# Kernel tuning notes

Measured on AMD Instinct MI355X. Metric: run time of the kernel, lower is better.

The kernel has to match this reference:

```python
import jax, jax.numpy as jnp
import numpy as np

D_MODEL = 1024
NUM_HEADS = 16
D_HEAD = D_MODEL // NUM_HEADS


def setup_inputs() -> dict:
    key = jax.random.key(0)
    ks = jax.random.split(key, 7)
    B, S = 2, 2048
    scale = 1.0 / np.sqrt(D_MODEL)
    return {
        "x": jax.random.normal(ks[0], (B, S, D_MODEL), dtype=jnp.float32),
        "attn_weights": jnp.zeros((1,), dtype=jnp.float32),  # unused in original forward
        "Wq": jax.random.normal(ks[1], (D_MODEL, D_MODEL), dtype=jnp.float32) * scale,
        "Wk": jax.random.normal(ks[2], (D_MODEL, D_MODEL), dtype=jnp.float32) * scale,
        "Wv": jax.random.normal(ks[3], (D_MODEL, D_MODEL), dtype=jnp.float32) * scale,
        "Wp": jax.random.normal(ks[4], (D_MODEL, D_MODEL), dtype=jnp.float32) * scale,
        "bp": jnp.zeros((D_MODEL,), dtype=jnp.float32),
    }


def reference(x, attn_weights, Wq, Wk, Wv, Wp, bp):
    B, S, D = x.shape
    H, Dh = NUM_HEADS, D_HEAD
    # torch Linear: y = x @ W.T  (weights stored [out, in])
    q = (x @ Wq.T).reshape(B, S, H, Dh).transpose(0, 2, 1, 3)  # [B,H,S,Dh]
    k = (x @ Wk.T).reshape(B, S, H, Dh).transpose(0, 2, 1, 3)
    v = (x @ Wv.T).reshape(B, S, H, Dh).transpose(0, 2, 1, 3)
    # NOTE: original module applies NO 1/sqrt(d) scaling
    scores = jnp.einsum("bhqd,bhkd->bhqk", q, k)
    weights = jax.nn.softmax(scores, axis=-1)  # dropout is inference no-op
    out = jnp.einsum("bhqk,bhkd->bhqd", weights, v)
    out = out.transpose(0, 2, 1, 3).reshape(B, S, D)
    return out @ Wp.T + bp
```

## Files before the change

### kernel.cpp

```cpp
#include <hip/hip_runtime.h>
#include <hip/hip_bf16.h>

#define D_MODEL 1024
#define NUM_HEADS 16
#define D_HEAD 64
#define BATCH 2
#define SEQ 2048
#define TOKENS (BATCH * SEQ)

typedef __attribute__((ext_vector_type(8))) short bf16x8;
typedef __attribute__((ext_vector_type(4))) float f32x4;
typedef __attribute__((ext_vector_type(2))) unsigned int uint2v;

typedef __attribute__((address_space(1))) const unsigned int as1_uint;
typedef __attribute__((address_space(3))) unsigned int as3_uint;

#define LOG2E 1.44269504088896340736f

static __device__ __forceinline__ unsigned short f2bf(float f) {
    unsigned int u = __builtin_bit_cast(unsigned int, f);
    u += 0x7fffu + ((u >> 16) & 1u);
    return (unsigned short)(u >> 16);
}

static __device__ __forceinline__ unsigned int pk2bf(float a, float b) {
    __hip_bfloat162 h = __float22bfloat162_rn(float2{a, b});
    unsigned int u;
    __builtin_memcpy(&u, &h, 4);
    return u;
}

static __device__ __forceinline__ float fast_exp2(float x) {
    return __builtin_amdgcn_exp2f(x);
}

__global__ __launch_bounds__(256) void convert_bf16(
    const float* __restrict__ x,  const float* __restrict__ Wq,
    const float* __restrict__ Wk, const float* __restrict__ Wv,
    const float* __restrict__ Wp,
    unsigned short* __restrict__ xb,  unsigned short* __restrict__ Wqb,
    unsigned short* __restrict__ Wkb, unsigned short* __restrict__ Wvb,
    unsigned short* __restrict__ Wpb)
{
    int v = blockIdx.x * 256 + threadIdx.x;
    const float* s;
    unsigned short* d;
    int off;
    if (v < (1 << 20)) { s = x; d = xb; off = v; }
    else {
        int u = v - (1 << 20);
        int w = u >> 18;
        off = u & ((1 << 18) - 1);
        s = (w == 0) ? Wq : (w == 1) ? Wk : (w == 2) ? Wv : Wp;
        d = (w == 0) ? Wqb : (w == 1) ? Wkb : (w == 2) ? Wvb : Wpb;
    }
    float4 f = ((const float4*)s)[off];
    ushort4 o = { f2bf(f.x), f2bf(f.y), f2bf(f.z), f2bf(f.w) };
    ((ushort4*)d)[off] = o;
}

__global__ __launch_bounds__(512) void qkv_gemm(
    const unsigned short* __restrict__ xb,
    const unsigned short* __restrict__ Wqb, const unsigned short* __restrict__ Wkb,
    const unsigned short* __restrict__ Wvb,
    unsigned short* __restrict__ Q, unsigned short* __restrict__ Kb,
    unsigned short* __restrict__ Vt)
{
    const int m0 = blockIdx.x * 128;
    const int n0 = blockIdx.y * 128;

    __shared__ __attribute__((aligned(16))) unsigned short sm[65536];

    const int t = threadIdx.x;
    const int wave = t >> 6, lane = t & 63;
    const int wm = (wave & 1) * 64, wn = (wave >> 1) * 32;
    const int l15 = lane & 15, quad = lane >> 4;
    const int sw = l15 & 7;

    const unsigned short* Wz[3] = { Wqb, Wkb, Wvb };

    f32x4 acc[3][4][2];
#pragma unroll
    for (int z = 0; z < 3; z++)
#pragma unroll
        for (int i = 0; i < 4; i++)
#pragma unroll
            for (int j = 0; j < 2; j++) acc[z][i][j] = (f32x4)0.f;

    auto stage = [&](int k0, int buf) {
#pragma unroll
        for (int i = 0; i < 2; i++) {
            int fbase = wave * 64 + i * 512;
            int f = fbase + lane;
            int row = f >> 3, cp = f & 7;
            int c = cp ^ (row & 7);
            int srcc = k0 + c * 8;
            __builtin_amdgcn_global_load_lds(
                (as1_uint*)&xb[(size_t)(m0 + row) * D_MODEL + srcc],
                (as3_uint*)&sm[buf * 32768 + fbase * 8], 16, 0, 0);
#pragma unroll
            for (int z = 0; z < 3; z++)
                __builtin_amdgcn_global_load_lds(
                    (as1_uint*)&Wz[z][(size_t)(n0 + row) * D_MODEL + srcc],
                    (as3_uint*)&sm[buf * 32768 + (1 + z) * 8192 + fbase * 8],
                    16, 0, 0);
        }
    };

    stage(0, 0);
    __syncthreads();

    int cur = 0;
    for (int k0 = 0; k0 < D_MODEL; k0 += 64) {
        if (k0 + 64 < D_MODEL) stage(k0 + 64, cur ^ 1);

        const unsigned short* lA = &sm[cur * 32768];
#pragma unroll
        for (int kk = 0; kk < 2; kk++) {
            const int cc = ((kk * 4 + quad) ^ sw) * 8;
            bf16x8 a[4];
#pragma unroll
            for (int mt = 0; mt < 4; mt++)
                a[mt] = *(const bf16x8*)&lA[(wm + mt * 16 + l15) * 64 + cc];
#pragma unroll
            for (int z = 0; z < 3; z++) {
                const unsigned short* lB = &sm[cur * 32768 + (1 + z) * 8192];
                bf16x8 b[2];
#pragma unroll
                for (int nt = 0; nt < 2; nt++)
                    b[nt] = *(const bf16x8*)&lB[(wn + nt * 16 + l15) * 64 + cc];
#pragma unroll
                for (int mt = 0; mt < 4; mt++)
#pragma unroll
                    for (int nt = 0; nt < 2; nt++)
                        acc[z][mt][nt] = __builtin_amdgcn_mfma_f32_16x16x32_bf16(
                            a[mt], b[nt], acc[z][mt][nt], 0, 0, 0);
            }
        }
        __syncthreads();
        cur ^= 1;
    }

#pragma unroll
    for (int mt = 0; mt < 4; mt++)
#pragma unroll
        for (int nt = 0; nt < 2; nt++)
#pragma unroll
            for (int r = 0; r < 4; r++) {
                int row = m0 + wm + mt * 16 + quad * 4 + r;
                int col = n0 + wn + nt * 16 + l15;
                Q[(size_t)row * D_MODEL + col]  = f2bf(acc[0][mt][nt][r] * LOG2E);
                Kb[(size_t)row * D_MODEL + col] = f2bf(acc[1][mt][nt][r]);
            }
    {
        const int b = m0 >> 11;
        const int srow = (m0 & 2047) + wm + quad * 4;
#pragma unroll
        for (int mt = 0; mt < 4; mt++)
#pragma unroll
            for (int nt = 0; nt < 2; nt++) {
                int col = n0 + wn + nt * 16 + l15;
                int h = col >> 6, dh = col & 63;
                ushort4 pk = { f2bf(acc[2][mt][nt][0]), f2bf(acc[2][mt][nt][1]),
                               f2bf(acc[2][mt][nt][2]), f2bf(acc[2][mt][nt][3]) };
                *(ushort4*)&Vt[(size_t)((b * 16 + h) * 64 + dh) * SEQ + srow + mt * 16] = pk;
            }
    }
}

__global__ __launch_bounds__(512, 4) void attn(
    const unsigned short* __restrict__ Q, const unsigned short* __restrict__ K,
    const unsigned short* __restrict__ Vt, unsigned short* __restrict__ O)
{
    const int q0 = blockIdx.x * 128;
    const int bh = blockIdx.y;
    const int b = bh >> 4, h = bh & 15;
    const size_t base = (size_t)b * SEQ * D_MODEL + (size_t)h * D_HEAD;
    const size_t baseV = (size_t)bh * D_HEAD * SEQ;

    __shared__ __attribute__((aligned(16))) char smem[40960];
    unsigned short* lK0 = (unsigned short*)&smem[0];
    unsigned short* lV0 = (unsigned short*)&smem[16384];

    const int t = threadIdx.x;
    const int wave = t >> 6, lane = t & 63;
    const int l15 = lane & 15, quad = lane >> 4;
    const int wq = wave & 3;
    const int sh = wave >> 2;
    const int qw = q0 + wq * 32;
    const int sbase = sh * (SEQ / 2);

    unsigned short* lK  = lK0 + sh * 4096;
    unsigned short* lVt = lV0 + sh * 4096;

    bf16x8 ones;
#pragma unroll
    for (int i = 0; i < 8; i++) ones[i] = (short)0x3F80;

    bf16x8 bq[2][2];
#pragma unroll
    for (int mq = 0; mq < 2; mq++)
#pragma unroll
        for (int kk = 0; kk < 2; kk++)
            bq[mq][kk] = *(const bf16x8*)&Q[base +
                (size_t)(qw + mq * 16 + l15) * D_MODEL + kk * 32 + quad * 8];

    const int tl = t & 255;
    const int r0 = tl >> 3, c0 = tl & 7;
    const int cs = (c0 ^ (r0 & 7)) * 8;
    const unsigned short* gK0 = &K[base + (size_t)(sbase + r0) * D_MODEL + c0 * 8];
    const unsigned short* gK1 = &K[base + (size_t)(sbase + r0 + 32) * D_MODEL + c0 * 8];
    const unsigned short* gV0 = &Vt[baseV + (size_t)r0 * SEQ + sbase + c0 * 8];
    const unsigned short* gV1 = &Vt[baseV + (size_t)(r0 + 32) * SEQ + sbase + c0 * 8];

    const int sw = l15 & 7;

    f32x4 o_acc[2][4];
#pragma unroll
    for (int i = 0; i < 2; i++)
#pragma unroll
        for (int j = 0; j < 4; j++) o_acc[i][j] = (f32x4)0.f;
    f32x4 o_l[2];
#pragma unroll
    for (int i = 0; i < 2; i++) o_l[i] = (f32x4)0.f;

    uint4 rK0 = *(const uint4*)gK0;
    uint4 rK1 = *(const uint4*)gK1;
    uint4 rV0 = *(const uint4*)gV0;
    uint4 rV1 = *(const uint4*)gV1;

    for (int s0 = 0; s0 < SEQ / 2; s0 += 64) {
        __syncthreads();
        *(uint4*)&lK[r0 * 64 + cs]        = rK0;
        *(uint4*)&lK[(r0 + 32) * 64 + cs] = rK1;
        *(uint4*)&lVt[r0 * 64 + cs]        = rV0;
        *(uint4*)&lVt[(r0 + 32) * 64 + cs] = rV1;
        __syncthreads();

        int sn = (s0 + 64 < SEQ / 2) ? s0 + 64 : 0;
        rK0 = *(const uint4*)(gK0 + (size_t)sn * D_MODEL);
        rK1 = *(const uint4*)(gK1 + (size_t)sn * D_MODEL);
        rV0 = *(const uint4*)(gV0 + sn);
        rV1 = *(const uint4*)(gV1 + sn);

        f32x4 st[4][2];
#pragma unroll
        for (int mt = 0; mt < 4; mt++)
#pragma unroll
            for (int mq = 0; mq < 2; mq++) st[mt][mq] = (f32x4)0.f;
#pragma unroll
        for (int kk = 0; kk < 2; kk++) {
            const int cc = ((kk * 4 + quad) ^ sw) * 8;
#pragma unroll
            for (int mt = 0; mt < 4; mt++) {
                bf16x8 ak = *(const bf16x8*)&lK[(mt * 16 + l15) * 64 + cc];
#pragma unroll
                for (int mq = 0; mq < 2; mq++)
                    st[mt][mq] = __builtin_amdgcn_mfma_f32_16x16x32_bf16(
                        ak, bq[mq][kk], st[mt][mq], 0, 0, 0);
            }
        }

#pragma unroll
        for (int mq = 0; mq < 2; mq++)
#pragma unroll
            for (int mt = 0; mt < 4; mt++)
#pragma unroll
                for (int r = 0; r < 4; r++)
                    st[mt][mq][r] = fast_exp2(st[mt][mq][r]);

        bf16x8 pa[2][2];
#pragma unroll
        for (int mq = 0; mq < 2; mq++)
#pragma unroll
            for (int kk = 0; kk < 2; kk++) {
                unsigned int cw[4];
#pragma unroll
                for (int j = 0; j < 2; j++) {
                    unsigned int w0 = pk2bf(st[2 * kk][mq][2 * j],
                                            st[2 * kk][mq][2 * j + 1]);
                    unsigned int w1 = pk2bf(st[2 * kk + 1][mq][2 * j],
                                            st[2 * kk + 1][mq][2 * j + 1]);
                    uint2v uv = __builtin_amdgcn_permlane32_swap(w0, w1, false, false);
                    uint2v f  = __builtin_amdgcn_permlane16_swap(uv[0], uv[1], false, false);
                    cw[j]     = f[0];
                    cw[2 + j] = f[1];
                }
                union { unsigned int w[4]; bf16x8 v; } u;
                u.w[0] = cw[0]; u.w[1] = cw[1]; u.w[2] = cw[2]; u.w[3] = cw[3];
                pa[mq][kk] = u.v;
            }

#pragma unroll
        for (int kk = 0; kk < 2; kk++) {
            const int cc = ((kk * 4 + quad) ^ sw) * 8;
            bf16x8 bv[4];
#pragma unroll
            for (int nt = 0; nt < 4; nt++)
                bv[nt] = *(const bf16x8*)&lVt[(nt * 16 + l15) * 64 + cc];
#pragma unroll
            for (int mq = 0; mq < 2; mq++) {
#pragma unroll
                for (int nt = 0; nt < 4; nt++)
                    o_acc[mq][nt] = __builtin_amdgcn_mfma_f32_16x16x32_bf16(
                        pa[mq][kk], bv[nt], o_acc[mq][nt], 0, 0, 0);
                o_l[mq] = __builtin_amdgcn_mfma_f32_16x16x32_bf16(
                    pa[mq][kk], ones, o_l[mq], 0, 0, 0);
            }
        }
    }

    float* sO = (float*)&smem[0];
    float* sL = (float*)&smem[36864];
    __syncthreads();
    if (sh == 1) {
#pragma unroll
        for (int mq = 0; mq < 2; mq++) {
#pragma unroll
            for (int r = 0; r < 4; r++)
                sL[wq * 32 + mq * 16 + quad * 4 + r] = o_l[mq][r];
#pragma unroll
            for (int nt = 0; nt < 4; nt++)
#pragma unroll
                for (int r = 0; r < 4; r++)
                    sO[(wq * 32 + mq * 16 + quad * 4 + r) * 68 + nt * 16 + l15] =
                        o_acc[mq][nt][r];
        }
    }
    __syncthreads();
    if (sh == 0) {
#pragma unroll
        for (int mq = 0; mq < 2; mq++) {
            float inv[4];
#pragma unroll
            for (int r = 0; r < 4; r++)
                inv[r] = 1.f / (o_l[mq][r] + sL[wq * 32 + mq * 16 + quad * 4 + r]);
#pragma unroll
            for (int nt = 0; nt < 4; nt++)
#pragma unroll
                for (int r = 0; r < 4; r++) {
                    int row = qw + mq * 16 + quad * 4 + r;
                    float v = o_acc[mq][nt][r] +
                              sO[(wq * 32 + mq * 16 + quad * 4 + r) * 68 + nt * 16 + l15];
                    O[base + (size_t)row * D_MODEL + nt * 16 + l15] = f2bf(v * inv[r]);
                }
        }
    }
}

__global__ __launch_bounds__(512) void proj_gemm(
    const unsigned short* __restrict__ A, const unsigned short* __restrict__ W,
    const float* __restrict__ bias, float* __restrict__ out)
{
    const int m0 = blockIdx.x * 128;
    const int n0 = blockIdx.y * 128;

    __shared__ __attribute__((aligned(16))) unsigned short lA[128 * 64];
    __shared__ __attribute__((aligned(16))) unsigned short lB[128 * 64];

    const int t = threadIdx.x;
    const int wave = t >> 6, lane = t & 63;
    const int wm = (wave & 1) * 64, wn = (wave >> 1) * 32;
    const int l15 = lane & 15, quad = lane >> 4;
    const int sw = l15 & 7;

    f32x4 acc[4][2];
#pragma unroll
    for (int i = 0; i < 4; i++)
#pragma unroll
        for (int j = 0; j < 2; j++) acc[i][j] = (f32x4)0.f;

    for (int k0 = 0; k0 < D_MODEL; k0 += 64) {
        __syncthreads();
#pragma unroll
        for (int i = 0; i < 2; i++) {
            int fbase = wave * 64 + i * 512;
            int f = fbase + lane;
            int row = f >> 3, cp = f & 7;
            int c = cp ^ (row & 7);
            __builtin_amdgcn_global_load_lds(
                (as1_uint*)&A[(size_t)(m0 + row) * D_MODEL + k0 + c * 8],
                (as3_uint*)&lA[fbase * 8], 16, 0, 0);
            __builtin_amdgcn_global_load_lds(
                (as1_uint*)&W[(size_t)(n0 + row) * D_MODEL + k0 + c * 8],
                (as3_uint*)&lB[fbase * 8], 16, 0, 0);
        }
        __syncthreads();

#pragma unroll
        for (int kk = 0; kk < 2; kk++) {
            const int cc = ((kk * 4 + quad) ^ sw) * 8;
            bf16x8 a[4], b[2];
#pragma unroll
            for (int mt = 0; mt < 4; mt++)
                a[mt] = *(const bf16x8*)&lA[(wm + mt * 16 + l15) * 64 + cc];
#pragma unroll
            for (int nt = 0; nt < 2; nt++)
                b[nt] = *(const bf16x8*)&lB[(wn + nt * 16 + l15) * 64 + cc];
#pragma unroll
            for (int mt = 0; mt < 4; mt++)
#pragma unroll
                for (int nt = 0; nt < 2; nt++)
                    acc[mt][nt] = __builtin_amdgcn_mfma_f32_16x16x32_bf16(
                        a[mt], b[nt], acc[mt][nt], 0, 0, 0);
        }
    }

#pragma unroll
    for (int mt = 0; mt < 4; mt++)
#pragma unroll
        for (int nt = 0; nt < 2; nt++)
#pragma unroll
            for (int r = 0; r < 4; r++) {
                int row = m0 + wm + mt * 16 + quad * 4 + r;
                int col = n0 + wn + nt * 16 + l15;
                out[(size_t)row * D_MODEL + col] = acc[mt][nt][r] + bias[col];
            }
}

extern "C" void kernel_launch(void* const* d_in, const int* in_sizes, int n_in,
                              void* d_out, int out_size, void* d_ws, size_t ws_size,
                              hipStream_t stream)
{
    const float* x  = (const float*)d_in[0];
    const float* Wq = (const float*)d_in[2];
    const float* Wk = (const float*)d_in[3];
    const float* Wv = (const float*)d_in[4];
    const float* Wp = (const float*)d_in[5];
    const float* bp = (const float*)d_in[6];
    float* out = (float*)d_out;

    unsigned short* Q   = (unsigned short*)d_ws;
    unsigned short* K   = Q   + (size_t)TOKENS * D_MODEL;
    unsigned short* Vt  = K   + (size_t)TOKENS * D_MODEL;
    unsigned short* O   = Vt  + (size_t)TOKENS * D_MODEL;
    unsigned short* xb  = O   + (size_t)TOKENS * D_MODEL;
    unsigned short* Wqb = xb  + (size_t)TOKENS * D_MODEL;
    unsigned short* Wkb = Wqb + (size_t)D_MODEL * D_MODEL;
    unsigned short* Wvb = Wkb + (size_t)D_MODEL * D_MODEL;
    unsigned short* Wpb = Wvb + (size_t)D_MODEL * D_MODEL;

    convert_bf16<<<8192, 256, 0, stream>>>(x, Wq, Wk, Wv, Wp,
                                           xb, Wqb, Wkb, Wvb, Wpb);
    qkv_gemm<<<dim3(TOKENS / 128, D_MODEL / 128), 512, 0, stream>>>(
        xb, Wqb, Wkb, Wvb, Q, K, Vt);
    attn<<<dim3(SEQ / 128, BATCH * NUM_HEADS), 512, 0, stream>>>(Q, K, Vt, O);
    proj_gemm<<<dim3(TOKENS / 128, D_MODEL / 128), 512, 0, stream>>>(O, Wpb, bp, out);
}
```

Baseline: 179.9 us.

## Halve GEMM N-tile to 64 and double-buffer proj_gemm loads

Both the QKV and output-projection GEMMs now use 128x64 tiles instead of 128x128. This doubles the grid to 512 blocks and cuts LDS and accumulator registers per block, so more blocks can fit on each CU (launch bounds of 4). proj_gemm also gets a double-buffered global_load_lds pipeline like qkv_gemm, which overlaps the next K-slice load with the current MFMAs. The trade-off is lower arithmetic intensity per block, so the A tile is reloaded twice as often.

```diff
diff --git a/kernel.cpp b/kernel.cpp
--- a/kernel.cpp
+++ b/kernel.cpp
@@ -59,7 +59,7 @@
     ((ushort4*)d)[off] = o;
 }
 
-__global__ __launch_bounds__(512) void qkv_gemm(
+__global__ __launch_bounds__(512, 4) void qkv_gemm(
     const unsigned short* __restrict__ xb,
     const unsigned short* __restrict__ Wqb, const unsigned short* __restrict__ Wkb,
     const unsigned short* __restrict__ Wvb,
@@ -67,25 +67,23 @@
     unsigned short* __restrict__ Vt)
 {
     const int m0 = blockIdx.x * 128;
-    const int n0 = blockIdx.y * 128;
-
-    __shared__ __attribute__((aligned(16))) unsigned short sm[65536];
+    const int n0 = blockIdx.y * 64;
+
+    __shared__ __attribute__((aligned(16))) unsigned short sm[40960];
 
     const int t = threadIdx.x;
     const int wave = t >> 6, lane = t & 63;
-    const int wm = (wave & 1) * 64, wn = (wave >> 1) * 32;
+    const int wm = (wave & 1) * 64, wn = (wave >> 1) * 16;
     const int l15 = lane & 15, quad = lane >> 4;
     const int sw = l15 & 7;
 
     const unsigned short* Wz[3] = { Wqb, Wkb, Wvb };
 
-    f32x4 acc[3][4][2];
+    f32x4 acc[3][4];
 #pragma unroll
     for (int z = 0; z < 3; z++)
 #pragma unroll
-        for (int i = 0; i < 4; i++)
-#pragma unroll
-            for (int j = 0; j < 2; j++) acc[z][i][j] = (f32x4)0.f;
+        for (int i = 0; i < 4; i++) acc[z][i] = (f32x4)0.f;
 
     auto stage = [&](int k0, int buf) {
 #pragma unroll
@@ -94,15 +92,19 @@
             int f = fbase + lane;
             int row = f >> 3, cp = f & 7;
             int c = cp ^ (row & 7);
-            int srcc = k0 + c * 8;
             __builtin_amdgcn_global_load_lds(
-                (as1_uint*)&xb[(size_t)(m0 + row) * D_MODEL + srcc],
-                (as3_uint*)&sm[buf * 32768 + fbase * 8], 16, 0, 0);
+                (as1_uint*)&xb[(size_t)(m0 + row) * D_MODEL + k0 + c * 8],
+                (as3_uint*)&sm[buf * 20480 + fbase * 8], 16, 0, 0);
+        }
+        {
+            int row = t >> 3, cp = t & 7;
+            int c = cp ^ (row & 7);
+            int fbase = wave * 64;
 #pragma unroll
             for (int z = 0; z < 3; z++)
                 __builtin_amdgcn_global_load_lds(
-                    (as1_uint*)&Wz[z][(size_t)(n0 + row) * D_MODEL + srcc],
-                    (as3_uint*)&sm[buf * 32768 + (1 + z) * 8192 + fbase * 8],
+                    (as1_uint*)&Wz[z][(size_t)(n0 + row) * D_MODEL + k0 + c * 8],
+                    (as3_uint*)&sm[buf * 20480 + 8192 + z * 4096 + fbase * 8],
                     16, 0, 0);
         }
     };
@@ -114,7 +116,7 @@
     for (int k0 = 0; k0 < D_MODEL; k0 += 64) {
         if (k0 + 64 < D_MODEL) stage(k0 + 64, cur ^ 1);
 
-        const unsigned short* lA = &sm[cur * 32768];
+        const unsigned short* lA = &sm[cur * 20480];
 #pragma unroll
         for (int kk = 0; kk < 2; kk++) {
             const int cc = ((kk * 4 + quad) ^ sw) * 8;
@@ -124,17 +126,12 @@
                 a[mt] = *(const bf16x8*)&lA[(wm + mt * 16 + l15) * 64 + cc];
 #pragma unroll
             for (int z = 0; z < 3; z++) {
-                const unsigned short* lB = &sm[cur * 32768 + (1 + z) * 8192];
-                bf16x8 b[2];
-#pragma unroll
-                for (int nt = 0; nt < 2; nt++)
-                    b[nt] = *(const bf16x8*)&lB[(wn + nt * 16 + l15) * 64 + cc];
+                const unsigned short* lB = &sm[cur * 20480 + 8192 + z * 4096];
+                bf16x8 b = *(const bf16x8*)&lB[(wn + l15) * 64 + cc];
 #pragma unroll
                 for (int mt = 0; mt < 4; mt++)
-#pragma unroll
-                    for (int nt = 0; nt < 2; nt++)
-                        acc[z][mt][nt] = __builtin_amdgcn_mfma_f32_16x16x32_bf16(
-                            a[mt], b[nt], acc[z][mt][nt], 0, 0, 0);
+                    acc[z][mt] = __builtin_amdgcn_mfma_f32_16x16x32_bf16(
+                        a[mt], b, acc[z][mt], 0, 0, 0);
             }
         }
         __syncthreads();
@@ -144,27 +141,23 @@
 #pragma unroll
     for (int mt = 0; mt < 4; mt++)
 #pragma unroll
-        for (int nt = 0; nt < 2; nt++)
-#pragma unroll
-            for (int r = 0; r < 4; r++) {
-                int row = m0 + wm + mt * 16 + quad * 4 + r;
-                int col = n0 + wn + nt * 16 + l15;
-                Q[(size_t)row * D_MODEL + col]  = f2bf(acc[0][mt][nt][r] * LOG2E);
-                Kb[(size_t)row * D_MODEL + col] = f2bf(acc[1][mt][nt][r]);
-            }
+        for (int r = 0; r < 4; r++) {
+            int row = m0 + wm + mt * 16 + quad * 4 + r;
+            int col = n0 + wn + l15;
+            Q[(size_t)row * D_MODEL + col]  = f2bf(acc[0][mt][r] * LOG2E);
+            Kb[(size_t)row * D_MODEL + col] = f2bf(acc[1][mt][r]);
+        }
     {
         const int b = m0 >> 11;
         const int srow = (m0 & 2047) + wm + quad * 4;
-#pragma unroll
-        for (int mt = 0; mt < 4; mt++)
-#pragma unroll
-            for (int nt = 0; nt < 2; nt++) {
-                int col = n0 + wn + nt * 16 + l15;
-                int h = col >> 6, dh = col & 63;
-                ushort4 pk = { f2bf(acc[2][mt][nt][0]), f2bf(acc[2][mt][nt][1]),
-                               f2bf(acc[2][mt][nt][2]), f2bf(acc[2][mt][nt][3]) };
-                *(ushort4*)&Vt[(size_t)((b * 16 + h) * 64 + dh) * SEQ + srow + mt * 16] = pk;
-            }
+        const int h = n0 >> 6;
+        const int dh = wn + l15;
+#pragma unroll
+        for (int mt = 0; mt < 4; mt++) {
+            ushort4 pk = { f2bf(acc[2][mt][0]), f2bf(acc[2][mt][1]),
+                           f2bf(acc[2][mt][2]), f2bf(acc[2][mt][3]) };
+            *(ushort4*)&Vt[(size_t)((b * 16 + h) * 64 + dh) * SEQ + srow + mt * 16] = pk;
+        }
     }
 }
 
@@ -348,30 +341,26 @@
     }
 }
 
-__global__ __launch_bounds__(512) void proj_gemm(
+__global__ __launch_bounds__(512, 4) void proj_gemm(
     const unsigned short* __restrict__ A, const unsigned short* __restrict__ W,
     const float* __restrict__ bias, float* __restrict__ out)
 {
     const int m0 = blockIdx.x * 128;
-    const int n0 = blockIdx.y * 128;
-
-    __shared__ __attribute__((aligned(16))) unsigned short lA[128 * 64];
-    __shared__ __attribute__((aligned(16))) unsigned short lB[128 * 64];
+    const int n0 = blockIdx.y * 64;
+
+    __shared__ __attribute__((aligned(16))) unsigned short sm[24576];
 
     const int t = threadIdx.x;
     const int wave = t >> 6, lane = t & 63;
-    const int wm = (wave & 1) * 64, wn = (wave >> 1) * 32;
+    const int wm = (wave & 1) * 64, wn = (wave >> 1) * 16;
     const int l15 = lane & 15, quad = lane >> 4;
     const int sw = l15 & 7;
 
-    f32x4 acc[4][2];
-#pragma unroll
-    for (int i = 0; i < 4; i++)
-#pragma unroll
-        for (int j = 0; j < 2; j++) acc[i][j] = (f32x4)0.f;
-
-    for (int k0 = 0; k0 < D_MODEL; k0 += 64) {
-        __syncthreads();
+    f32x4 acc[4];
+#pragma unroll
+    for (int i = 0; i < 4; i++) acc[i] = (f32x4)0.f;
+
+    auto stage = [&](int k0, int buf) {
 #pragma unroll
         for (int i = 0; i < 2; i++) {
             int fbase = wave * 64 + i * 512;
@@ -380,42 +369,53 @@
             int c = cp ^ (row & 7);
             __builtin_amdgcn_global_load_lds(
                 (as1_uint*)&A[(size_t)(m0 + row) * D_MODEL + k0 + c * 8],
-                (as3_uint*)&lA[fbase * 8], 16, 0, 0);
+                (as3_uint*)&sm[buf * 12288 + fbase * 8], 16, 0, 0);
+        }
+        {
+            int row = t >> 3, cp = t & 7;
+            int c = cp ^ (row & 7);
+            int fbase = wave * 64;
             __builtin_amdgcn_global_load_lds(
                 (as1_uint*)&W[(size_t)(n0 + row) * D_MODEL + k0 + c * 8],
-                (as3_uint*)&lB[fbase * 8], 16, 0, 0);
-        }
-        __syncthreads();
-
+                (as3_uint*)&sm[buf * 12288 + 8192 + fbase * 8], 16, 0, 0);
+        }
+    };
+
+    stage(0, 0);
+    __syncthreads();
+
+    int cur = 0;
+    for (int k0 = 0; k0 < D_MODEL; k0 += 64) {
+        if (k0 + 64 < D_MODEL) stage(k0 + 64, cur ^ 1);
+
+        const unsigned short* lA = &sm[cur * 12288];
+        const unsigned short* lB = &sm[cur * 12288 + 8192];
 #pragma unroll
         for (int kk = 0; kk < 2; kk++) {
             const int cc = ((kk * 4 + quad) ^ sw) * 8;
-            bf16x8 a[4], b[2];
+            bf16x8 a[4];
 #pragma unroll
             for (int mt = 0; mt < 4; mt++)
                 a[mt] = *(const bf16x8*)&lA[(wm + mt * 16 + l15) * 64 + cc];
-#pragma unroll
-            for (int nt = 0; nt < 2; nt++)
-                b[nt] = *(const bf16x8*)&lB[(wn + nt * 16 + l15) * 64 + cc];
+            bf16x8 b = *(const bf16x8*)&lB[(wn + l15) * 64 + cc];
 #pragma unroll
             for (int mt = 0; mt < 4; mt++)
-#pragma unroll
-                for (int nt = 0; nt < 2; nt++)
-                    acc[mt][nt] = __builtin_amdgcn_mfma_f32_16x16x32_bf16(
-                        a[mt], b[nt], acc[mt][nt], 0, 0, 0);
-        }
-    }
-
+                acc[mt] = __builtin_amdgcn_mfma_f32_16x16x32_bf16(
+                    a[mt], b, acc[mt], 0, 0, 0);
+        }
+        __syncthreads();
+        cur ^= 1;
+    }
+
+    const int col = n0 + wn + l15;
+    const float bc = bias[col];
 #pragma unroll
     for (int mt = 0; mt < 4; mt++)
 #pragma unroll
-        for (int nt = 0; nt < 2; nt++)
-#pragma unroll
-            for (int r = 0; r < 4; r++) {
-                int row = m0 + wm + mt * 16 + quad * 4 + r;
-                int col = n0 + wn + nt * 16 + l15;
-                out[(size_t)row * D_MODEL + col] = acc[mt][nt][r] + bias[col];
-            }
+        for (int r = 0; r < 4; r++) {
+            int row = m0 + wm + mt * 16 + quad * 4 + r;
+            out[(size_t)row * D_MODEL + col] = acc[mt][r] + bc;
+        }
 }
 
 extern "C" void kernel_launch(void* const* d_in, const int* in_sizes, int n_in,
@@ -442,8 +442,8 @@
 
     convert_bf16<<<8192, 256, 0, stream>>>(x, Wq, Wk, Wv, Wp,
                                            xb, Wqb, Wkb, Wvb, Wpb);
-    qkv_gemm<<<dim3(TOKENS / 128, D_MODEL / 128), 512, 0, stream>>>(
+    qkv_gemm<<<dim3(TOKENS / 128, D_MODEL / 64), 512, 0, stream>>>(
         xb, Wqb, Wkb, Wvb, Q, K, Vt);
     attn<<<dim3(SEQ / 128, BATCH * NUM_HEADS), 512, 0, stream>>>(Q, K, Vt, O);
-    proj_gemm<<<dim3(TOKENS / 128, D_MODEL / 128), 512, 0, stream>>>(O, Wpb, bp, out);
-}
+    proj_gemm<<<dim3(TOKENS / 128, D_MODEL / 64), 512, 0, stream>>>(O, Wpb, bp, out);
+}
```

After: 170.1 us. -5.4%, faster.
